# Kernel optimization log

Hardware: AMD Instinct MI355X
Metric: run time of the kernel (lower is better)

## Reference

```python
import jax, jax.numpy as jnp
import numpy as np

EMBED_DIM = 512
NUM_HEADS = 8
GLOBAL_MIX = 0.5


def setup_inputs() -> dict:
    key = jax.random.key(0)
    ks = jax.random.split(key, 7)
    B, L, E = 8, 1024, EMBED_DIM
    s = 1.0 / np.sqrt(E)
    x = jax.random.normal(ks[0], (B, L, E), dtype=jnp.float32)
    mask = jax.random.randint(ks[1], (B, L), 0, 2) > 0  # True = valid token
    Wq = jax.random.normal(ks[2], (E, E), dtype=jnp.float32) * s
    Wk = jax.random.normal(ks[3], (E, E), dtype=jnp.float32) * s
    Wv = jax.random.normal(ks[4], (E, E), dtype=jnp.float32) * s
    Wo = jax.random.normal(ks[5], (E, E), dtype=jnp.float32) * s
    G = jax.random.normal(ks[6], (L, L), dtype=jnp.float32)
    return {"x": x, "mask": mask, "Wq": Wq, "Wk": Wk, "Wv": Wv, "Wo": Wo, "G": G}


def _tanh_mha(x, mask, Wq, Wk, Wv, Wo, G):
    B, L, E = x.shape
    H = NUM_HEADS
    D = E // H
    scale = 1.0 / np.sqrt(D)
    dt = x.dtype
    fmax = jnp.finfo(dt).max
    tiny = jnp.finfo(dt).tiny

    def split_heads(t):  # (B,L,E) -> (B,H,L,D)
        return t.reshape(B, L, H, D).transpose(0, 2, 1, 3)

    q = split_heads(x @ Wq.T)
    k = split_heads(x @ Wk.T)
    v = split_heads(x @ Wv.T)

    scores = jnp.tanh(jnp.einsum('bhqd,bhkd->bhqk', q, k) * scale)
    key_valid = mask[:, None, None, :]  # (B,1,1,L)
    scores = jnp.where(key_valid, scores, -jnp.inf)

    finite = jnp.isfinite(scores)
    finite_scores = jnp.where(finite, scores, -fmax)
    m = jnp.max(finite_scores, axis=(1, 2, 3), keepdims=True)  # per-sample amax over heads+q+k
    m = jnp.where(jnp.isfinite(m), m, jnp.zeros_like(m))
    exp_scores = jnp.where(finite, jnp.exp(scores - m), jnp.zeros_like(scores))

    mf = mask.astype(dt)
    exp_scores = exp_scores * mf[:, None, None, :] * mf[:, None, :, None]
    denom = jnp.maximum(exp_scores.sum(axis=(1, 2, 3), keepdims=True), tiny)
    weights = exp_scores / denom
    # dropout p=0 -> identity; renorm pass kept for faithfulness
    renorm = jnp.maximum(weights.sum(axis=(1, 2, 3), keepdims=True), tiny)
    weights = weights / renorm

    # learnable global attention: softmax rows, clamp, mask, normalize over (q,k)
    activated = jnp.maximum(jax.nn.softmax(G, axis=-1), 0.0)  # (L,L)
    gscores = activated[None] * mf[:, None, :] * mf[:, :, None]  # (B,L,L)
    gsums = jnp.maximum(gscores.sum(axis=(1, 2), keepdims=True), tiny)
    gnorm = (gscores / gsums)[:, None]  # (B,1,L,L)
    weights = (1.0 - GLOBAL_MIX) * weights + GLOBAL_MIX * gnorm

    attended = jnp.einsum('bhqk,bhkd->bhqd', weights, v)
    attended = attended * mf[:, None, :, None]
    attended = attended.transpose(0, 2, 1, 3).reshape(B, L, E)
    return attended @ Wo.T


def reference(x, mask, Wq, Wk, Wv, Wo, G):
    return _tanh_mha(x, mask, Wq, Wk, Wv, Wo, G)
```

## Files before the change

### kernel.cpp

```cpp
#include <hip/hip_runtime.h>
#include <math.h>

#define B_ 8
#define L_ 1024
#define E_ 512
#define H_ 8
#define D_ 64
#define QSZ (B_*H_*L_*D_)
#define BLE ((size_t)B_*L_*E_)
#define TINYF 1.175494350822287508e-38f
#define SWK(r) ((((r) ^ ((r) >> 3))) & 7)

typedef unsigned short u16;
typedef __attribute__((ext_vector_type(8))) short bfrag;
typedef __attribute__((ext_vector_type(4))) float ffrag;
typedef __attribute__((ext_vector_type(16))) float ffrag16;
typedef __attribute__((ext_vector_type(4))) short vshort4;

#if __has_builtin(__builtin_amdgcn_exp2f)
#define EXP2F(x) __builtin_amdgcn_exp2f(x)
#else
#define EXP2F(x) __expf((x) * 0.6931471805599453f)
#endif
#if __has_builtin(__builtin_amdgcn_rcpf)
#define RCPF(x) __builtin_amdgcn_rcpf(x)
#else
#define RCPF(x) (1.0f / (x))
#endif

__device__ __forceinline__ u16 f2b(float f) {
  unsigned u = __float_as_uint(f);
  u += 0x7fffu + ((u >> 16) & 1u);
  return (u16)(u >> 16);
}
__device__ __forceinline__ unsigned pk2(float a, float b) {
  unsigned ua = __float_as_uint(a); ua += 0x7fffu + ((ua >> 16) & 1u);
  unsigned ub = __float_as_uint(b); ub += 0x7fffu + ((ub >> 16) & 1u);
  return (ua >> 16) | (ub & 0xffff0000u);
}
__device__ __forceinline__ float blo(unsigned u) { return __uint_as_float(u << 16); }
__device__ __forceinline__ float bhi(unsigned u) { return __uint_as_float(u & 0xffff0000u); }

__device__ __forceinline__ bfrag cvt8v(const float* __restrict__ src) {
  float4 a = *(const float4*)src;
  float4 b = *(const float4*)(src + 4);
  bfrag r;
  r[0]=(short)f2b(a.x); r[1]=(short)f2b(a.y); r[2]=(short)f2b(a.z); r[3]=(short)f2b(a.w);
  r[4]=(short)f2b(b.x); r[5]=(short)f2b(b.y); r[6]=(short)f2b(b.z); r[7]=(short)f2b(b.w);
  return r;
}

__device__ __forceinline__ void gll16(const void* g, void* l) {
  __builtin_amdgcn_global_load_lds(
      (const __attribute__((address_space(1))) void*)g,
      (__attribute__((address_space(3))) void*)l, 16, 0, 0);
}

__global__ __launch_bounds__(256) void prep_k(
    const float* __restrict__ x, const float* __restrict__ Wq,
    const float* __restrict__ Wk, const float* __restrict__ Wv,
    const float* __restrict__ Wo, const int* __restrict__ mask,
    u16* __restrict__ xb, u16* __restrict__ Wb,
    int* __restrict__ posb, int* __restrict__ nvb, int* __restrict__ itok,
    float* __restrict__ sums) {
  const int bid = blockIdx.x, t = threadIdx.x;
  __shared__ int sc[256];
  if (bid < 2048) {
    size_t c = (size_t)bid * 256 + t;
    *(bfrag*)&xb[c * 8] = cvt8v(x + c * 8);
    return;
  }
  if (bid < 2560) {
    const int c2 = bid - 2048;
    const float* src = (c2 < 128) ? Wq : (c2 < 256) ? Wk : (c2 < 384) ? Wv : Wo;
    const size_t base = (size_t)(c2 >> 7) * 262144;
    const size_t cc = (size_t)(c2 & 127) * 256 + t;
    *(bfrag*)&Wb[base + cc * 8] = cvt8v(src + cc * 8);
    return;
  }
  const int bb = bid - 2560;
  int4 mi = *(const int4*)(mask + bb * 1024 + t * 4);
  const int vx = mi.x ? 1 : 0, vy = mi.y ? 1 : 0;
  const int vz = mi.z ? 1 : 0, vw = mi.w ? 1 : 0;
  const int c0 = vx + vy + vz + vw;
  sc[t] = c0;
  __syncthreads();
#pragma unroll
  for (int off = 1; off < 256; off <<= 1) {
    int v = (t >= off) ? sc[t - off] : 0;
    __syncthreads();
    sc[t] += v;
    __syncthreads();
  }
  const int nvtot = sc[255];
  int pv = sc[t] - c0;
  int pi = t * 4 - pv;
  int4 pq;
  pq.x = vx ? pv : nvtot + pi; pv += vx; pi += 1 - vx;
  pq.y = vy ? pv : nvtot + pi; pv += vy; pi += 1 - vy;
  pq.z = vz ? pv : nvtot + pi; pv += vz; pi += 1 - vz;
  pq.w = vw ? pv : nvtot + pi;
  *(int4*)(posb + bb * 1024 + t * 4) = pq;
  itok[bb * 1024 + pq.x] = t * 4;
  itok[bb * 1024 + pq.y] = t * 4 + 1;
  itok[bb * 1024 + pq.z] = t * 4 + 2;
  itok[bb * 1024 + pq.w] = t * 4 + 3;
  if (t == 0) { nvb[bb] = nvtot; sums[bb] = 0.0f; }
}

__global__ __launch_bounds__(256) void proj_k(
    const u16* __restrict__ xb, const u16* __restrict__ Wb,
    const float* __restrict__ G, const int* __restrict__ mask,
    const int* __restrict__ nvb, const int* __restrict__ itok,
    u16* __restrict__ actb, float* __restrict__ R,
    u16* __restrict__ Qb, u16* __restrict__ Kb, u16* __restrict__ Vtb) {
  const int bid = blockIdx.x, t = threadIdx.x;
  __shared__ __align__(16) u16 As[128 * 64];
  __shared__ __align__(16) u16 Bs[128 * 64];
  __shared__ float sred[8];
  __shared__ float rred[4][8];
  const int w = t >> 6, lane = t & 63;

  if (bid < 1024) {
    const int q = bid;
    float4 g4 = ((const float4*)(G + (size_t)q * 1024))[t];
    float m = fmaxf(fmaxf(g4.x, g4.y), fmaxf(g4.z, g4.w));
#pragma unroll
    for (int off = 32; off > 0; off >>= 1) m = fmaxf(m, __shfl_down(m, off));
    if (lane == 0) sred[w] = m;
    __syncthreads();
    m = fmaxf(fmaxf(sred[0], sred[1]), fmaxf(sred[2], sred[3]));
    float e0 = __expf(g4.x - m), e1 = __expf(g4.y - m);
    float e2 = __expf(g4.z - m), e3 = __expf(g4.w - m);
    float s = e0 + e1 + e2 + e3;
#pragma unroll
    for (int off = 32; off > 0; off >>= 1) s += __shfl_down(s, off);
    if (lane == 0) sred[4 + w] = s;
    __syncthreads();
    const float inv = 1.0f / (sred[4] + sred[5] + sred[6] + sred[7]);
    const unsigned p0 = pk2(e0 * inv, e1 * inv);
    const unsigned p1 = pk2(e2 * inv, e3 * inv);
    *(uint2*)&actb[(size_t)q * 1024 + t * 4] = make_uint2(p0, p1);
    const float r0 = blo(p0), r1 = bhi(p0);
    const float r2 = blo(p1), r3 = bhi(p1);
    float rd[8];
#pragma unroll
    for (int b = 0; b < 8; ++b) {
      const int* mkp = mask + b * 1024 + t * 4;
      rd[b] = (mkp[0] ? r0 : 0.f) + (mkp[1] ? r1 : 0.f) +
              (mkp[2] ? r2 : 0.f) + (mkp[3] ? r3 : 0.f);
#pragma unroll
      for (int off = 32; off > 0; off >>= 1) rd[b] += __shfl_down(rd[b], off);
    }
    if (lane == 0)
#pragma unroll
      for (int b = 0; b < 8; ++b) rred[w][b] = rd[b];
    __syncthreads();
    if (t < 8) R[q * 8 + t] = rred[0][t] + rred[1][t] + rred[2][t] + rred[3][t];
    return;
  }

  const int gid = bid - 1024;
  const int m0 = (gid & 63) * 128;
  const int n0 = (gid >> 6) * 128;
  const int l15 = lane & 15, quad = lane >> 4;
  const int mq = (w >> 1) * 64, nq = (w & 1) * 64;
  const int z = n0 >> 9;
  const int b = m0 >> 10, q0c = m0 & 1023;

  int tokr[4];
  if (z == 0) {
    const int nv = nvb[b];
    if (q0c >= nv) return;
    const int* it = itok + b * 1024;
#pragma unroll
    for (int j = 0; j < 4; ++j) {
      const int c = w * 256 + j * 64 + lane;
      tokr[j] = b * 1024 + it[q0c + (c >> 3)];
    }
  } else {
#pragma unroll
    for (int j = 0; j < 4; ++j) {
      const int c = w * 256 + j * 64 + lane;
      tokr[j] = m0 + (c >> 3);
    }
  }

  const ffrag fz = {0.f, 0.f, 0.f, 0.f};
  ffrag acc[4][4];
#pragma unroll
  for (int i = 0; i < 4; ++i)
#pragma unroll
    for (int j = 0; j < 4; ++j) acc[i][j] = fz;

  for (int kk = 0; kk < 512; kk += 64) {
    __syncthreads();
#pragma unroll
    for (int j = 0; j < 4; ++j) {
      const int c = w * 256 + j * 64 + lane;
      const int row = c >> 3, ck = (c & 7) ^ (row & 7);
      gll16(xb + (size_t)tokr[j] * 512 + kk + ck * 8,
            &As[(size_t)(w * 256 + j * 64) * 8]);
    }
#pragma unroll
    for (int j = 0; j < 4; ++j) {
      const int c = w * 256 + j * 64 + lane;
      const int row = c >> 3, ck = (c & 7) ^ (row & 7);
      gll16(Wb + (size_t)(n0 + row) * 512 + kk + ck * 8,
            &Bs[(size_t)(w * 256 + j * 64) * 8]);
    }
    __syncthreads();
#pragma unroll
    for (int s = 0; s < 2; ++s) {
      bfrag av[4], bv[4];
#pragma unroll
      for (int i = 0; i < 4; ++i) {
        const int ar = mq + i * 16 + l15;
        av[i] = *(const bfrag*)&As[ar * 64 + (((quad + 4 * s) ^ (ar & 7)) << 3)];
        const int br = nq + i * 16 + l15;
        bv[i] = *(const bfrag*)&Bs[br * 64 + (((quad + 4 * s) ^ (br & 7)) << 3)];
      }
#pragma unroll
      for (int i = 0; i < 4; ++i)
#pragma unroll
        for (int j = 0; j < 4; ++j)
          acc[i][j] = __builtin_amdgcn_mfma_f32_16x16x32_bf16(av[i], bv[j], acc[i][j], 0, 0, 0);
    }
  }
  const int c0 = n0 & 511;
#pragma unroll
  for (int i = 0; i < 4; ++i) {
    const int mbase = m0 + mq + i * 16 + quad * 4;
    const int l0 = mbase & 1023;
#pragma unroll
    for (int j = 0; j < 4; ++j) {
      const int nc = c0 + nq + j * 16 + l15;
      const int h = nc >> 6, d = nc & 63;
      if (z == 0) {
        u16* dst = Qb + ((size_t)(b * 8 + h) * 1024 + l0) * 64 + d;
#pragma unroll
        for (int r = 0; r < 4; ++r) dst[(size_t)r * 64] = f2b(acc[i][j][r]);
      } else if (z == 1) {
        u16* dst = Kb + ((size_t)(b * 8 + h) * 1024 + l0) * 64 + d;
#pragma unroll
        for (int r = 0; r < 4; ++r) dst[(size_t)r * 64] = f2b(acc[i][j][r]);
      } else {
        vshort4 vs;
#pragma unroll
        for (int r = 0; r < 4; ++r)
          vs[r] = (short)(mask[b * 1024 + l0 + r] ? f2b(acc[i][j][r]) : (u16)0);
        *(vshort4*)(Vtb + ((size_t)(b * 8 + h) * 64 + d) * 1024 + l0) = vs;
      }
    }
  }
}

__global__ __launch_bounds__(256) void attn_gv_k(
    const u16* __restrict__ Qb, const u16* __restrict__ Kb,
    const u16* __restrict__ Vtb, const u16* __restrict__ actb,
    const int* __restrict__ mask, const int* __restrict__ nvb,
    const int* __restrict__ itok, const float* __restrict__ R,
    u16* __restrict__ AEb, u16* __restrict__ AGb, float* __restrict__ denom) {
  __shared__ __align__(16) u16 POOL[13320];
  const int t = threadIdx.x, w = t >> 6, lane = t & 63;
  const int l15 = lane & 15, quad = lane >> 4;

  if (blockIdx.x == 1536) {
    float* rr = (float*)POOL;
    float a8[8] = {0,0,0,0,0,0,0,0};
    for (int q = t; q < 1024; q += 256)
#pragma unroll
      for (int b = 0; b < 8; ++b)
        if (mask[b * 1024 + q]) a8[b] += R[q * 8 + b];
#pragma unroll
    for (int b = 0; b < 8; ++b) {
#pragma unroll
      for (int off = 32; off > 0; off >>= 1) a8[b] += __shfl_down(a8[b], off);
    }
    if (lane == 0)
#pragma unroll
      for (int b = 0; b < 8; ++b) rr[w * 8 + b] = a8[b];
    __syncthreads();
    if (t < 8) denom[8 + t] = rr[t] + rr[8 + t] + rr[16 + t] + rr[24 + t];
    return;
  }

  const int X = blockIdx.x & 7;
  const int s = blockIdx.x >> 3;
  const int s3 = s % 3, sd3 = s / 3;

  if (s3 == 2) {
    u16* As = POOL;
    u16* Bs = POOL + 4096;
    const int b = X;
    const int q0 = (sd3 >> 2) * 64;
    const int n0 = (sd3 & 3) * 128;
    const int nv = nvb[b];
    if (q0 >= nv) return;
    const int* it = itok + b * 1024;
    const int m0 = b * 1024 + q0;
    const int mq = (w >> 1) * 32, nq = (w & 1) * 64;
    const ffrag fz = {0.f, 0.f, 0.f, 0.f};
    ffrag acc[2][4];
#pragma unroll
    for (int i = 0; i < 2; ++i)
#pragma unroll
      for (int j = 0; j < 4; ++j) acc[i][j] = fz;

    int tokr[2];
#pragma unroll
    for (int j = 0; j < 2; ++j) {
      const int c = w * 128 + j * 64 + lane;
      tokr[j] = it[q0 + (c >> 3)];
    }

    for (int kk = 0; kk < 1024; kk += 64) {
      __syncthreads();
#pragma unroll
      for (int j = 0; j < 2; ++j) {
        const int c = w * 128 + j * 64 + lane;
        const int row = c >> 3, ck = (c & 7) ^ (row & 7);
        gll16(actb + (size_t)tokr[j] * 1024 + kk + ck * 8,
              &As[(size_t)(w * 128 + j * 64) * 8]);
      }
#pragma unroll
      for (int j = 0; j < 4; ++j) {
        const int c = w * 256 + j * 64 + lane;
        const int row = c >> 3, ck = (c & 7) ^ (row & 7);
        gll16(Vtb + (size_t)(b * 512 + n0 + row) * 1024 + kk + ck * 8,
              &Bs[(size_t)(w * 256 + j * 64) * 8]);
      }
      __syncthreads();
#pragma unroll
      for (int sgm = 0; sgm < 2; ++sgm) {
        bfrag av[2], bv[4];
#pragma unroll
        for (int i = 0; i < 2; ++i) {
          const int ar = mq + i * 16 + l15;
          av[i] = *(const bfrag*)&As[ar * 64 + (((quad + 4 * sgm) ^ (ar & 7)) << 3)];
        }
#pragma unroll
        for (int j = 0; j < 4; ++j) {
          const int br = nq + j * 16 + l15;
          bv[j] = *(const bfrag*)&Bs[br * 64 + (((quad + 4 * sgm) ^ (br & 7)) << 3)];
        }
#pragma unroll
        for (int i = 0; i < 2; ++i)
#pragma unroll
          for (int j = 0; j < 4; ++j)
            acc[i][j] = __builtin_amdgcn_mfma_f32_16x16x32_bf16(av[i], bv[j], acc[i][j], 0, 0, 0);
      }
    }
#pragma unroll
    for (int i = 0; i < 2; ++i) {
      const int mbase = m0 + mq + i * 16 + quad * 4;
#pragma unroll
      for (int j = 0; j < 4; ++j) {
        const int n = n0 + nq + j * 16 + l15;
#pragma unroll
        for (int r = 0; r < 4; ++r)
          AGb[(size_t)(mbase + r) * 512 + n] = f2b(acc[i][j][r]);
      }
    }
    return;
  }

  const int a_ = sd3 * 2 + s3;
  const int qt = a_ & 15;
  const int h = a_ >> 4;
  const int b = X;
  const int bh = X * 8 + h;
  const int nv = nvb[b];
  if (qt * 64 >= nv) return;
  u16* Ks = POOL;
  u16* Vs = POOL + 4096;
  u16* Es = POOL + 8192;
  u16* Ms = POOL + 12288;
  float* red4 = (float*)(POOL + 13312);
  const int l31 = lane & 31, hi = lane >> 5;
  const int qsb = w >> 1, msb = w & 1;
  const int qpb = w & 1, dpb = w >> 1;

  const u16* Kg = Kb + (size_t)bh * 65536;
  const u16* Vg = Vtb + (size_t)bh * 65536;

  const u16* Qrow = Qb + ((size_t)bh * 1024 + qt * 64 + qsb * 32 + l31) * 64;
  bfrag qf[4];
#pragma unroll
  for (int ko = 0; ko < 4; ++ko) qf[ko] = *(const bfrag*)(Qrow + ko * 16 + hi * 8);

  {
    int4 mi = *(const int4*)(mask + b * 1024 + t * 4);
    vshort4 mv;
    mv[0] = mi.x ? (short)0x3F80 : (short)0; mv[1] = mi.y ? (short)0x3F80 : (short)0;
    mv[2] = mi.z ? (short)0x3F80 : (short)0; mv[3] = mi.w ? (short)0x3F80 : (short)0;
    *(vshort4*)&Ms[t * 4] = mv;
  }

  auto stageK = [&](int kt) {
#pragma unroll
    for (int j = 0; j < 2; ++j) {
      const int c = w * 128 + j * 64 + lane;
      const int row = c >> 3, ck = (c & 7) ^ SWK(row);
      gll16(Kg + (size_t)(kt * 64 + row) * 64 + ck * 8,
            &Ks[(size_t)(w * 128 + j * 64) * 8]);
    }
  };
  auto stageV = [&](int kt) {
#pragma unroll
    for (int j = 0; j < 2; ++j) {
      const int c = w * 128 + j * 64 + lane;
      const int row = c >> 3, ck = (c & 7) ^ SWK(row);
      gll16(Vg + (size_t)row * 1024 + kt * 64 + ck * 8,
            &Vs[(size_t)(w * 128 + j * 64) * 8]);
    }
  };

  stageK(0); stageV(0);
  __syncthreads();

  ffrag16 accE, dacc;
#pragma unroll
  for (int i = 0; i < 16; ++i) { accE[i] = 0.f; dacc[i] = 0.f; }

  for (int kt = 0; kt < 16; ++kt) {
    ffrag16 st;
#pragma unroll
    for (int i = 0; i < 16; ++i) st[i] = 0.f;
    const int krow = msb * 32 + l31;
    const int kk7 = SWK(krow);
#pragma unroll
    for (int ko = 0; ko < 4; ++ko) {
      bfrag ak = *(const bfrag*)&Ks[krow * 64 + (((ko * 2 + hi) ^ kk7) << 3)];
      st = __builtin_amdgcn_mfma_f32_32x32x16_bf16(ak, qf[ko], st, 0, 0, 0);
    }
    const int qrow = qsb * 32 + l31;
    const int qk7 = SWK(qrow);
#pragma unroll
    for (int g = 0; g < 4; ++g) {
      float ee[4];
#pragma unroll
      for (int r = 0; r < 4; ++r) {
        const float tt = EXP2F(st[4 * g + r] * 0.360673760222f);
        ee[r] = EXP2F(RCPF(tt + 1.0f) * -2.88539008178f);
      }
      const int k0 = msb * 32 + g * 8 + hi * 4;
      *(uint2*)&Es[qrow * 64 + (((k0 >> 3) ^ qk7) << 3) + (k0 & 7)] =
          make_uint2(pk2(ee[0], ee[1]), pk2(ee[2], ee[3]));
    }
    __syncthreads();
    if (kt < 15) stageK(kt + 1);

    const int erow = qpb * 32 + l31;
    const int ek7 = SWK(erow);
    const int vrow = dpb * 32 + l31;
    const int vk7 = SWK(vrow);
#pragma unroll
    for (int ko = 0; ko < 4; ++ko) {
      const int co = ko * 2 + hi;
      bfrag ea = *(const bfrag*)&Es[erow * 64 + ((co ^ ek7) << 3)];
      bfrag bv = *(const bfrag*)&Vs[vrow * 64 + ((co ^ vk7) << 3)];
      accE = __builtin_amdgcn_mfma_f32_32x32x16_bf16(ea, bv, accE, 0, 0, 0);
      if (dpb == 0) {
        bfrag bm = *(const bfrag*)&Ms[kt * 64 + ko * 16 + hi * 8];
        dacc = __builtin_amdgcn_mfma_f32_32x32x16_bf16(ea, bm, dacc, 0, 0, 0);
      }
    }
    __syncthreads();
    if (kt < 15) stageV(kt + 1);
  }

  const size_t obase = ((size_t)(b * 1024 + qt * 64 + qpb * 32)) * 512
                       + h * 64 + dpb * 32 + l31;
#pragma unroll
  for (int r = 0; r < 16; ++r) {
    const int qloc = (r & 3) + 8 * (r >> 2) + 4 * hi;
    AEb[obase + (size_t)qloc * 512] = f2b(accE[r]);
  }
  float dsumv = 0.0f;
  if (l31 == 0 && dpb == 0) {
    const int cq0 = qt * 64 + qpb * 32 + 4 * hi;
#pragma unroll
    for (int r = 0; r < 16; ++r) {
      const int cq = cq0 + (r & 3) + 8 * (r >> 2);
      dsumv += (cq < nv) ? dacc[r] : 0.0f;
    }
    red4[qpb * 2 + hi] = dsumv;
  }
  __syncthreads();
  if (t == 0) atomicAdd(denom + b, red4[0] + red4[1] + red4[2] + red4[3]);
}

__global__ __launch_bounds__(256) void o_proj_k(
    const u16* __restrict__ AEb, const u16* __restrict__ AGb,
    const int* __restrict__ nvb, const int* __restrict__ itok,
    const float* __restrict__ sums,
    const u16* __restrict__ Wb, float* __restrict__ out) {
  const int m0 = blockIdx.x * 128;
  const int n0 = blockIdx.y * 128;
  const int b = m0 >> 10;
  const int q0c = m0 & 1023;
  const int nv = nvb[b];
  const int* it = itok + b * 1024;
  const int t = threadIdx.x, w = t >> 6, lane = t & 63;

  if (q0c >= nv) {
    const int row = q0c + (t >> 1);
    const int tok = it[row];
    float4 z4 = make_float4(0.f, 0.f, 0.f, 0.f);
    float* dst = out + ((size_t)(b * 1024 + tok)) * 512 + n0 + (t & 1) * 64;
#pragma unroll
    for (int i = 0; i < 16; ++i) *(float4*)(dst + i * 4) = z4;
    return;
  }

  const float c1 = 0.5f / fmaxf(sums[b], TINYF);
  const float c2 = 0.5f / fmaxf(sums[8 + b], TINYF);
  __shared__ __align__(16) u16 As[128 * 64];
  __shared__ __align__(16) u16 Bs[128 * 64];
  const int l15 = lane & 15, quad = lane >> 4;
  const int mq = (w >> 1) * 64, nq = (w & 1) * 64;

  const ffrag fz = {0.f, 0.f, 0.f, 0.f};
  ffrag acc[4][4];
#pragma unroll
  for (int i = 0; i < 4; ++i)
#pragma unroll
    for (int j = 0; j < 4; ++j) acc[i][j] = fz;

  for (int kk = 0; kk < 512; kk += 64) {
    __syncthreads();
#pragma unroll
    for (int i = 0; i < 4; ++i) {
      const int c = t + i * 256;
      const int row = c >> 3, ck = c & 7;
      const size_t gofs = (size_t)(b * 1024 + q0c + row) * 512 + kk + ck * 8;
      uint4 ua = *(const uint4*)(AEb + gofs);
      uint4 ug = *(const uint4*)(AGb + gofs);
      const int valid = (q0c + row) < nv;
      const float a1 = valid ? c1 : 0.0f, a2 = valid ? c2 : 0.0f;
      uint4 res;
      res.x = pk2(a1 * blo(ua.x) + a2 * blo(ug.x), a1 * bhi(ua.x) + a2 * bhi(ug.x));
      res.y = pk2(a1 * blo(ua.y) + a2 * blo(ug.y), a1 * bhi(ua.y) + a2 * bhi(ug.y));
      res.z = pk2(a1 * blo(ua.z) + a2 * blo(ug.z), a1 * bhi(ua.z) + a2 * bhi(ug.z));
      res.w = pk2(a1 * blo(ua.w) + a2 * blo(ug.w), a1 * bhi(ua.w) + a2 * bhi(ug.w));
      *(uint4*)&As[row * 64 + ((ck ^ (row & 7)) << 3)] = res;
    }
#pragma unroll
    for (int j = 0; j < 4; ++j) {
      const int c = w * 256 + j * 64 + lane;
      const int row = c >> 3, ck = (c & 7) ^ (row & 7);
      gll16(Wb + (size_t)(1536 + n0 + row) * 512 + kk + ck * 8,
            &Bs[(size_t)(w * 256 + j * 64) * 8]);
    }
    __syncthreads();
#pragma unroll
    for (int s = 0; s < 2; ++s) {
      bfrag av[4], bv[4];
#pragma unroll
      for (int i = 0; i < 4; ++i) {
        const int ar = mq + i * 16 + l15;
        av[i] = *(const bfrag*)&As[ar * 64 + (((quad + 4 * s) ^ (ar & 7)) << 3)];
        const int br = nq + i * 16 + l15;
        bv[i] = *(const bfrag*)&Bs[br * 64 + (((quad + 4 * s) ^ (br & 7)) << 3)];
      }
#pragma unroll
      for (int i = 0; i < 4; ++i)
#pragma unroll
        for (int j = 0; j < 4; ++j)
          acc[i][j] = __builtin_amdgcn_mfma_f32_16x16x32_bf16(av[i], bv[j], acc[i][j], 0, 0, 0);
    }
  }
#pragma unroll
  for (int i = 0; i < 4; ++i) {
    const int crow0 = q0c + mq + i * 16 + quad * 4;
    const int4 tk = *(const int4*)(it + crow0);
#pragma unroll
    for (int j = 0; j < 4; ++j) {
      const int n = n0 + nq + j * 16 + l15;
      out[(size_t)(b * 1024 + tk.x) * 512 + n] = (crow0     < nv) ? acc[i][j][0] : 0.0f;
      out[(size_t)(b * 1024 + tk.y) * 512 + n] = (crow0 + 1 < nv) ? acc[i][j][1] : 0.0f;
      out[(size_t)(b * 1024 + tk.z) * 512 + n] = (crow0 + 2 < nv) ? acc[i][j][2] : 0.0f;
      out[(size_t)(b * 1024 + tk.w) * 512 + n] = (crow0 + 3 < nv) ? acc[i][j][3] : 0.0f;
    }
  }
}

extern "C" void kernel_launch(void* const* d_in, const int* in_sizes, int n_in,
                              void* d_out, int out_size, void* d_ws, size_t ws_size,
                              hipStream_t stream) {
  const float* x  = (const float*)d_in[0];
  const int* mask = (const int*)d_in[1];
  const float* Wq = (const float*)d_in[2];
  const float* Wk = (const float*)d_in[3];
  const float* Wv = (const float*)d_in[4];
  const float* Wo = (const float*)d_in[5];
  const float* G  = (const float*)d_in[6];
  float* out = (float*)d_out;

  u16* xb   = (u16*)d_ws;
  u16* Wb   = xb + (size_t)8192 * 512;
  u16* Qb   = Wb + (size_t)2048 * 512;
  u16* Kb   = Qb + QSZ;
  u16* Vtb  = Kb + QSZ;
  u16* actb = Vtb + QSZ;
  u16* AEb  = actb + (size_t)1024 * 1024;
  u16* AGb  = AEb + BLE;
  float* R  = (float*)(AGb + BLE);
  float* SUMS = R + 8192;
  int* posb = (int*)(SUMS + 16);
  int* nvb  = posb + 8192;
  int* itok = nvb + 8;

  prep_k<<<2568, 256, 0, stream>>>(x, Wq, Wk, Wv, Wo, mask, xb, Wb, posb, nvb, itok, SUMS);
  proj_k<<<1792, 256, 0, stream>>>(xb, Wb, G, mask, nvb, itok, actb, R, Qb, Kb, Vtb);
  attn_gv_k<<<1537, 256, 0, stream>>>(Qb, Kb, Vtb, actb, mask, nvb, itok, R, AEb, AGb, SUMS);
  o_proj_k<<<dim3(64, 4), 256, 0, stream>>>(AEb, AGb, nvb, itok, SUMS, Wb, out);
}
```

Baseline: 171.2 us.

## Compact tokens for K/V and global attention to skip masked keys

Projects K and V only for valid tokens in compacted order and scatters the global softmax matrix into a per-batch compacted layout (8 copies instead of one shared). Attention and global-mix loops now run only over ceil(nv/64) key tiles rather than all 1024, with key validity derived from position rather than from the mask. This removes work on masked keys in the projection, attention and G·V GEMMs. The cost is an 8x larger scattered write of the global matrix and more scattered stores in proj_k.

```diff
diff --git a/kernel.cpp b/kernel.cpp
--- a/kernel.cpp
+++ b/kernel.cpp
@@ -40,6 +40,7 @@
 }
 __device__ __forceinline__ float blo(unsigned u) { return __uint_as_float(u << 16); }
 __device__ __forceinline__ float bhi(unsigned u) { return __uint_as_float(u & 0xffff0000u); }
+__device__ __forceinline__ float b2f(u16 v) { return __uint_as_float((unsigned)v << 16); }
 
 __device__ __forceinline__ bfrag cvt8v(const float* __restrict__ src) {
   float4 a = *(const float4*)src;
@@ -111,8 +112,9 @@
 __global__ __launch_bounds__(256) void proj_k(
     const u16* __restrict__ xb, const u16* __restrict__ Wb,
     const float* __restrict__ G, const int* __restrict__ mask,
-    const int* __restrict__ nvb, const int* __restrict__ itok,
-    u16* __restrict__ actb, float* __restrict__ R,
+    const int* __restrict__ posb, const int* __restrict__ nvb,
+    const int* __restrict__ itok,
+    u16* __restrict__ actc, float* __restrict__ R,
     u16* __restrict__ Qb, u16* __restrict__ Kb, u16* __restrict__ Vtb) {
   const int bid = blockIdx.x, t = threadIdx.x;
   __shared__ __align__(16) u16 As[128 * 64];
@@ -138,17 +140,22 @@
     if (lane == 0) sred[4 + w] = s;
     __syncthreads();
     const float inv = 1.0f / (sred[4] + sred[5] + sred[6] + sred[7]);
-    const unsigned p0 = pk2(e0 * inv, e1 * inv);
-    const unsigned p1 = pk2(e2 * inv, e3 * inv);
-    *(uint2*)&actb[(size_t)q * 1024 + t * 4] = make_uint2(p0, p1);
-    const float r0 = blo(p0), r1 = bhi(p0);
-    const float r2 = blo(p1), r3 = bhi(p1);
+    const u16 a0 = f2b(e0 * inv), a1 = f2b(e1 * inv);
+    const u16 a2 = f2b(e2 * inv), a3 = f2b(e3 * inv);
+    const float r0 = b2f(a0), r1 = b2f(a1), r2 = b2f(a2), r3 = b2f(a3);
     float rd[8];
 #pragma unroll
     for (int b = 0; b < 8; ++b) {
-      const int* mkp = mask + b * 1024 + t * 4;
-      rd[b] = (mkp[0] ? r0 : 0.f) + (mkp[1] ? r1 : 0.f) +
-              (mkp[2] ? r2 : 0.f) + (mkp[3] ? r3 : 0.f);
+      const int4 mi = *(const int4*)(mask + b * 1024 + t * 4);
+      const int4 pk = *(const int4*)(posb + b * 1024 + t * 4);
+      const int rowc = posb[b * 1024 + q];
+      u16* dst = actc + ((size_t)b << 20) + ((size_t)rowc << 10);
+      dst[pk.x] = mi.x ? a0 : (u16)0;
+      dst[pk.y] = mi.y ? a1 : (u16)0;
+      dst[pk.z] = mi.z ? a2 : (u16)0;
+      dst[pk.w] = mi.w ? a3 : (u16)0;
+      rd[b] = (mi.x ? r0 : 0.f) + (mi.y ? r1 : 0.f) +
+              (mi.z ? r2 : 0.f) + (mi.w ? r3 : 0.f);
 #pragma unroll
       for (int off = 32; off > 0; off >>= 1) rd[b] += __shfl_down(rd[b], off);
     }
@@ -167,23 +174,14 @@
   const int mq = (w >> 1) * 64, nq = (w & 1) * 64;
   const int z = n0 >> 9;
   const int b = m0 >> 10, q0c = m0 & 1023;
-
+  const int nv = nvb[b];
+  if (q0c >= nv) return;
+  const int* it = itok + b * 1024;
   int tokr[4];
-  if (z == 0) {
-    const int nv = nvb[b];
-    if (q0c >= nv) return;
-    const int* it = itok + b * 1024;
-#pragma unroll
-    for (int j = 0; j < 4; ++j) {
-      const int c = w * 256 + j * 64 + lane;
-      tokr[j] = b * 1024 + it[q0c + (c >> 3)];
-    }
-  } else {
-#pragma unroll
-    for (int j = 0; j < 4; ++j) {
-      const int c = w * 256 + j * 64 + lane;
-      tokr[j] = m0 + (c >> 3);
-    }
+#pragma unroll
+  for (int j = 0; j < 4; ++j) {
+    const int c = w * 256 + j * 64 + lane;
+    tokr[j] = b * 1024 + it[q0c + (c >> 3)];
   }
 
   const ffrag fz = {0.f, 0.f, 0.f, 0.f};
@@ -248,7 +246,7 @@
         vshort4 vs;
 #pragma unroll
         for (int r = 0; r < 4; ++r)
-          vs[r] = (short)(mask[b * 1024 + l0 + r] ? f2b(acc[i][j][r]) : (u16)0);
+          vs[r] = (short)((l0 + r < nv) ? f2b(acc[i][j][r]) : (u16)0);
         *(vshort4*)(Vtb + ((size_t)(b * 8 + h) * 64 + d) * 1024 + l0) = vs;
       }
     }
@@ -257,11 +255,11 @@
 
 __global__ __launch_bounds__(256) void attn_gv_k(
     const u16* __restrict__ Qb, const u16* __restrict__ Kb,
-    const u16* __restrict__ Vtb, const u16* __restrict__ actb,
+    const u16* __restrict__ Vtb, const u16* __restrict__ actc,
     const int* __restrict__ mask, const int* __restrict__ nvb,
-    const int* __restrict__ itok, const float* __restrict__ R,
+    const float* __restrict__ R,
     u16* __restrict__ AEb, u16* __restrict__ AGb, float* __restrict__ denom) {
-  __shared__ __align__(16) u16 POOL[13320];
+  __shared__ __align__(16) u16 POOL[12296];
   const int t = threadIdx.x, w = t >> 6, lane = t & 63;
   const int l15 = lane & 15, quad = lane >> 4;
 
@@ -297,8 +295,9 @@
     const int n0 = (sd3 & 3) * 128;
     const int nv = nvb[b];
     if (q0 >= nv) return;
-    const int* it = itok + b * 1024;
+    const int kkmax = (nv + 63) & ~63;
     const int m0 = b * 1024 + q0;
+    const u16* actg = actc + ((size_t)b << 20);
     const int mq = (w >> 1) * 32, nq = (w & 1) * 64;
     const ffrag fz = {0.f, 0.f, 0.f, 0.f};
     ffrag acc[2][4];
@@ -307,20 +306,13 @@
 #pragma unroll
       for (int j = 0; j < 4; ++j) acc[i][j] = fz;
 
-    int tokr[2];
-#pragma unroll
-    for (int j = 0; j < 2; ++j) {
-      const int c = w * 128 + j * 64 + lane;
-      tokr[j] = it[q0 + (c >> 3)];
-    }
-
-    for (int kk = 0; kk < 1024; kk += 64) {
+    for (int kk = 0; kk < kkmax; kk += 64) {
       __syncthreads();
 #pragma unroll
       for (int j = 0; j < 2; ++j) {
         const int c = w * 128 + j * 64 + lane;
         const int row = c >> 3, ck = (c & 7) ^ (row & 7);
-        gll16(actb + (size_t)tokr[j] * 1024 + kk + ck * 8,
+        gll16(actg + (size_t)(q0 + row) * 1024 + kk + ck * 8,
               &As[(size_t)(w * 128 + j * 64) * 8]);
       }
 #pragma unroll
@@ -372,11 +364,11 @@
   const int bh = X * 8 + h;
   const int nv = nvb[b];
   if (qt * 64 >= nv) return;
+  const int ktmax = (nv + 63) >> 6;
   u16* Ks = POOL;
   u16* Vs = POOL + 4096;
   u16* Es = POOL + 8192;
-  u16* Ms = POOL + 12288;
-  float* red4 = (float*)(POOL + 13312);
+  float* red4 = (float*)(POOL + 12288);
   const int l31 = lane & 31, hi = lane >> 5;
   const int qsb = w >> 1, msb = w & 1;
   const int qpb = w & 1, dpb = w >> 1;
@@ -388,14 +380,6 @@
   bfrag qf[4];
 #pragma unroll
   for (int ko = 0; ko < 4; ++ko) qf[ko] = *(const bfrag*)(Qrow + ko * 16 + hi * 8);
-
-  {
-    int4 mi = *(const int4*)(mask + b * 1024 + t * 4);
-    vshort4 mv;
-    mv[0] = mi.x ? (short)0x3F80 : (short)0; mv[1] = mi.y ? (short)0x3F80 : (short)0;
-    mv[2] = mi.z ? (short)0x3F80 : (short)0; mv[3] = mi.w ? (short)0x3F80 : (short)0;
-    *(vshort4*)&Ms[t * 4] = mv;
-  }
 
   auto stageK = [&](int kt) {
 #pragma unroll
@@ -423,7 +407,7 @@
 #pragma unroll
   for (int i = 0; i < 16; ++i) { accE[i] = 0.f; dacc[i] = 0.f; }
 
-  for (int kt = 0; kt < 16; ++kt) {
+  for (int kt = 0; kt < ktmax; ++kt) {
     ffrag16 st;
 #pragma unroll
     for (int i = 0; i < 16; ++i) st[i] = 0.f;
@@ -439,17 +423,18 @@
 #pragma unroll
     for (int g = 0; g < 4; ++g) {
       float ee[4];
+      const int kq = kt * 64 + msb * 32 + g * 8 + hi * 4;
 #pragma unroll
       for (int r = 0; r < 4; ++r) {
         const float tt = EXP2F(st[4 * g + r] * 0.360673760222f);
-        ee[r] = EXP2F(RCPF(tt + 1.0f) * -2.88539008178f);
+        ee[r] = (kq + r < nv) ? EXP2F(RCPF(tt + 1.0f) * -2.88539008178f) : 0.0f;
       }
       const int k0 = msb * 32 + g * 8 + hi * 4;
       *(uint2*)&Es[qrow * 64 + (((k0 >> 3) ^ qk7) << 3) + (k0 & 7)] =
           make_uint2(pk2(ee[0], ee[1]), pk2(ee[2], ee[3]));
     }
     __syncthreads();
-    if (kt < 15) stageK(kt + 1);
+    if (kt < ktmax - 1) stageK(kt + 1);
 
     const int erow = qpb * 32 + l31;
     const int ek7 = SWK(erow);
@@ -462,12 +447,16 @@
       bfrag bv = *(const bfrag*)&Vs[vrow * 64 + ((co ^ vk7) << 3)];
       accE = __builtin_amdgcn_mfma_f32_32x32x16_bf16(ea, bv, accE, 0, 0, 0);
       if (dpb == 0) {
-        bfrag bm = *(const bfrag*)&Ms[kt * 64 + ko * 16 + hi * 8];
+        const int kbase = kt * 64 + ko * 16 + hi * 8;
+        bfrag bm;
+#pragma unroll
+        for (int jj = 0; jj < 8; ++jj)
+          bm[jj] = (short)((kbase + jj < nv) ? 0x3F80 : 0);
         dacc = __builtin_amdgcn_mfma_f32_32x32x16_bf16(ea, bm, dacc, 0, 0, 0);
       }
     }
     __syncthreads();
-    if (kt < 15) stageV(kt + 1);
+    if (kt < ktmax - 1) stageV(kt + 1);
   }
 
   const size_t obase = ((size_t)(b * 1024 + qt * 64 + qpb * 32)) * 512
@@ -534,10 +523,11 @@
     for (int i = 0; i < 4; ++i) {
       const int c = t + i * 256;
       const int row = c >> 3, ck = c & 7;
-      const size_t gofs = (size_t)(b * 1024 + q0c + row) * 512 + kk + ck * 8;
+      const int valid = (q0c + row) < nv;
+      const int rowr = valid ? (q0c + row) : 0;
+      const size_t gofs = (size_t)(b * 1024 + rowr) * 512 + kk + ck * 8;
       uint4 ua = *(const uint4*)(AEb + gofs);
       uint4 ug = *(const uint4*)(AGb + gofs);
-      const int valid = (q0c + row) < nv;
       const float a1 = valid ? c1 : 0.0f, a2 = valid ? c2 : 0.0f;
       uint4 res;
       res.x = pk2(a1 * blo(ua.x) + a2 * blo(ug.x), a1 * bhi(ua.x) + a2 * bhi(ug.x));
@@ -603,8 +593,8 @@
   u16* Qb   = Wb + (size_t)2048 * 512;
   u16* Kb   = Qb + QSZ;
   u16* Vtb  = Kb + QSZ;
-  u16* actb = Vtb + QSZ;
-  u16* AEb  = actb + (size_t)1024 * 1024;
+  u16* actc = Vtb + QSZ;
+  u16* AEb  = actc + ((size_t)8 << 20);
   u16* AGb  = AEb + BLE;
   float* R  = (float*)(AGb + BLE);
   float* SUMS = R + 8192;
@@ -613,7 +603,7 @@
   int* itok = nvb + 8;
 
   prep_k<<<2568, 256, 0, stream>>>(x, Wq, Wk, Wv, Wo, mask, xb, Wb, posb, nvb, itok, SUMS);
-  proj_k<<<1792, 256, 0, stream>>>(xb, Wb, G, mask, nvb, itok, actb, R, Qb, Kb, Vtb);
-  attn_gv_k<<<1537, 256, 0, stream>>>(Qb, Kb, Vtb, actb, mask, nvb, itok, R, AEb, AGb, SUMS);
+  proj_k<<<1792, 256, 0, stream>>>(xb, Wb, G, mask, posb, nvb, itok, actc, R, Qb, Kb, Vtb);
+  attn_gv_k<<<1537, 256, 0, stream>>>(Qb, Kb, Vtb, actc, mask, nvb, R, AEb, AGb, SUMS);
   o_proj_k<<<dim3(64, 4), 256, 0, stream>>>(AEb, AGb, nvb, itok, SUMS, Wb, out);
 }
```

New measurement: 159.2 us. -7.0%, faster.
